# Kernel optimization log

Measured on AMD Instinct MI355X. Metric: run time of the kernel, lower is better.

Reference implementation:

```python
import jax, jax.numpy as jnp
import numpy as np

N_NODES = 50000


def rgcn_conv(x, src, dst, edge_type, W, root, bias):
    """PyG RGCNConv: out[i] = x[i] @ root + bias + sum_r mean_{j in N_r(i)} x[j] @ W[r].
    W: [R, F_in, F_out]. Mean aggregation is per-relation (PyG default aggr='mean')."""
    num_rel = W.shape[0]
    n = x.shape[0]
    out = x @ root + bias
    x_src = x[src]  # [E, F_in] gather once
    for r in range(num_rel):  # small fixed relation count
        mask = (edge_type == r)
        msg = jnp.where(mask[:, None], x_src, 0.0) @ W[r]          # [E, F_out]
        s = jax.ops.segment_sum(msg, dst, num_segments=n)           # [N, F_out]
        c = jax.ops.segment_sum(mask.astype(x.dtype), dst, num_segments=n)  # [N]
        out = out + s / jnp.maximum(c, 1.0)[:, None]
    return out


def setup_inputs() -> dict:
    key = jax.random.key(0)
    ks = jax.random.split(key, 10)
    N, E, F_in, F_hid, F_out, R = N_NODES, 800000, 128, 128, 64, 8
    x = jax.random.normal(ks[0], (N, F_in), dtype=jnp.float32)
    edge_index = jax.random.randint(ks[1], (2, E), 0, N, dtype=jnp.int64)
    edge_type = jax.random.randint(ks[2], (E,), 0, R, dtype=jnp.int64)
    s1 = 1.0 / np.sqrt(F_in)
    s2 = 1.0 / np.sqrt(F_hid)
    W1 = jax.random.normal(ks[3], (R, F_in, F_hid), dtype=jnp.float32) * s1
    root1 = jax.random.normal(ks[4], (F_in, F_hid), dtype=jnp.float32) * s1
    b1 = jnp.zeros((F_hid,), dtype=jnp.float32)
    W2 = jax.random.normal(ks[5], (R, F_hid, F_out), dtype=jnp.float32) * s2
    root2 = jax.random.normal(ks[6], (F_hid, F_out), dtype=jnp.float32) * s2
    b2 = jnp.zeros((F_out,), dtype=jnp.float32)
    return {"x": x, "edge_index": edge_index, "edge_type": edge_type,
            "W1": W1, "root1": root1, "b1": b1,
            "W2": W2, "root2": root2, "b2": b2}


def reference(x, edge_index, edge_type, W1, root1, b1, W2, root2, b2):
    src, dst = edge_index[0], edge_index[1]
    h = jax.nn.relu(rgcn_conv(x, src, dst, edge_type, W1, root1, b1))
    out = rgcn_conv(h, src, dst, edge_type, W2, root2, b2)
    return out
```

## Files before the change

kernel.cpp:

```cpp
#include <hip/hip_runtime.h>

#define N_NODES 50000
#define N_EDGES 800000
#define R_REL   8

#define TNBKT   3125
#define TCAP    512
#define SLAB    4096
#define BINBLK  ((N_EDGES + SLAB - 1) / SLAB)

typedef float  f32x4  __attribute__((ext_vector_type(4)));
typedef __bf16 bf16x8 __attribute__((ext_vector_type(8)));

__device__ __forceinline__ unsigned short f2bf(float f) {
    unsigned int u = __float_as_uint(f);
    u = (u + 0x7FFFu + ((u >> 16) & 1u)) >> 16;
    return (unsigned short)u;
}
__device__ __forceinline__ float bflo(unsigned int u) { return __uint_as_float(u << 16); }
__device__ __forceinline__ float bfhi(unsigned int u) { return __uint_as_float(u & 0xFFFF0000u); }

__device__ __forceinline__ void acc16(float* a, uint4 u0, uint4 u1) {
    a[0]  += bflo(u0.x);   a[1]  += bfhi(u0.x);
    a[2]  += bflo(u0.y);   a[3]  += bfhi(u0.y);
    a[4]  += bflo(u0.z);   a[5]  += bfhi(u0.z);
    a[6]  += bflo(u0.w);   a[7]  += bfhi(u0.w);
    a[8]  += bflo(u1.x);   a[9]  += bfhi(u1.x);
    a[10] += bflo(u1.y);   a[11] += bfhi(u1.y);
    a[12] += bflo(u1.z);   a[13] += bfhi(u1.z);
    a[14] += bflo(u1.w);   a[15] += bfhi(u1.w);
}


#define W1_ELEMS (9 * 128 * 128)
#define W2_ELEMS (9 * 64 * 128)
#define N4       (N_NODES * 32)
#define NB_CVT   ((N4 + 255) / 256)
#define NB_PREP  (BINBLK + NB_CVT)

__global__ __launch_bounds__(256) void k_prep(
    const int* __restrict__ src, const int* __restrict__ dst,
    const int* __restrict__ et, int* __restrict__ gcur,
    unsigned* __restrict__ gbin,
    const float* __restrict__ x, unsigned short* __restrict__ xb,
    const float* __restrict__ root1, const float* __restrict__ W1,
    const float* __restrict__ root2, const float* __restrict__ W2,
    unsigned short* __restrict__ Wt1, unsigned short* __restrict__ Wt2)
{
    __shared__ int hist[TNBKT];
    __shared__ int base[TNBKT];
    const int t = threadIdx.x;

    if (blockIdx.x < BINBLK) {
        const int e0 = blockIdx.x * SLAB;
        for (int i = t; i < TNBKT; i += 256) hist[i] = 0;
        __syncthreads();
#pragma unroll
        for (int i = 0; i < SLAB / 256; ++i) {
            int e = e0 + i * 256 + t;
            if (e < N_EDGES) atomicAdd(&hist[dst[e] >> 4], 1);
        }
        __syncthreads();
        for (int i = t; i < TNBKT; i += 256) {
            int h = hist[i];
            base[i] = (h > 0) ? atomicAdd(&gcur[i], h) : 0;
            hist[i] = 0;
        }
        __syncthreads();
#pragma unroll
        for (int i = 0; i < SLAB / 256; ++i) {
            int e = e0 + i * 256 + t;
            if (e < N_EDGES) {
                int d = dst[e];
                int b = d >> 4;
                int sub = atomicAdd(&hist[b], 1);
                int pos = base[b] + sub;
                unsigned rec = ((unsigned)src[e] << 7) | (unsigned)((d & 15) * 8 + et[e]);
                if (pos < TCAP) gbin[(size_t)b * TCAP + pos] = rec;
            }
        }
        return;
    }

    const int idx = (blockIdx.x - BINBLK) * 256 + t;
    if (idx < N4) {
        float4 v = *(const float4*)(x + (size_t)idx * 4);
        ushort4 o;
        o.x = f2bf(v.x); o.y = f2bf(v.y); o.z = f2bf(v.z); o.w = f2bf(v.w);
        *(ushort4*)(xb + (size_t)idx * 4) = o;
    }
    if (idx < W1_ELEMS) {
        int j    = idx & 7;
        int lane = (idx >> 3) & 63;
        int r    = idx >> 9;
        int nb   = r & 7;
        int r2   = r >> 3;
        int kk   = r2 & 3;
        int seg  = r2 >> 2;
        int k = kk * 32 + (lane >> 4) * 8 + j;
        int n = nb * 16 + (lane & 15);
        float v = (seg == 0) ? root1[k * 128 + n] : W1[((seg - 1) * 128 + k) * 128 + n];
        Wt1[idx] = f2bf(v);
    } else if (idx < W1_ELEMS + W2_ELEMS) {
        int i2   = idx - W1_ELEMS;
        int j    = i2 & 7;
        int lane = (i2 >> 3) & 63;
        int r    = i2 >> 9;
        int nb   = r & 3;
        int r2   = r >> 2;
        int kk   = r2 & 3;
        int seg  = r2 >> 2;
        int k = kk * 32 + (lane >> 4) * 8 + j;
        int n = nb * 16 + (lane & 15);
        float v = (seg == 0) ? root2[k * 64 + n] : W2[((seg - 1) * 128 + k) * 64 + n];
        Wt2[i2] = f2bf(v);
    }
}


template <int FOUT, bool RELU, bool OUT_BF16>
__global__ __launch_bounds__(512) void k_fused(
    const unsigned short* __restrict__ xin,
    const unsigned short* __restrict__ WtP,
    const float* __restrict__ bias,
    const int* __restrict__ gcnt,
    const unsigned* __restrict__ gbin,
    unsigned short* __restrict__ outb,
    float* __restrict__ outf)
{
    constexpr int NBt = FOUT / 16;
    __shared__ __align__(16) unsigned short As0[16][136];
    __shared__ __align__(16) unsigned short As[8][16][136];
    __shared__ unsigned short sorted[TCAP];
    __shared__ int dcnt[128];
    __shared__ int kbeg[128];
    __shared__ int kcur[128];

    const int t = threadIdx.x;
    const int node0 = blockIdx.x * 16;

    if (t < 128) { dcnt[t] = 0; kcur[t] = 0; }
    if (t < 128) {
        const int sr = t >> 3;
        const int sp = t & 7;
        const uint4* s4 = (const uint4*)(xin + (size_t)(node0 + sr) * 128 + sp * 16);
        uint4 r0 = s4[0], r1 = s4[1];
        uint4* d = (uint4*)&As0[sr][sp * 16];
        d[0] = r0; d[1] = r1;
    }
    const int nraw = gcnt[blockIdx.x];
    const int n = nraw < TCAP ? nraw : TCAP;
    unsigned rec = 0;
    if (t < n) rec = gbin[(size_t)blockIdx.x * TCAP + t];
    __syncthreads();

    if (t < n) atomicAdd(&dcnt[rec & 127], 1);
    __syncthreads();

    if (t < 64) {
        int d0 = dcnt[2 * t], d1 = dcnt[2 * t + 1];
        int s = d0 + d1;
        int inc = s;
#pragma unroll
        for (int off = 1; off < 64; off <<= 1) {
            int y = __shfl_up(inc, off, 64);
            if (t >= off) inc += y;
        }
        int excl = inc - s;
        kbeg[2 * t]     = excl;
        kbeg[2 * t + 1] = excl + d0;
    }
    __syncthreads();

    if (t < n) {
        int key = rec & 127;
        int pos = atomicAdd(&kcur[key], 1);
        sorted[kbeg[key] + pos] = (unsigned short)(rec >> 7);
    }
    __syncthreads();

    {
        const int key = t >> 2;
        const int q   = t & 3;
        const int rel = key & 7;
        const int nl  = key >> 3;

        const int beg = kbeg[key];
        const int deg = dcnt[key];
        const int end = beg + deg;

        const unsigned short* bx = xin + q * 32;
        float a[32];
#pragma unroll
        for (int i = 0; i < 32; ++i) a[i] = 0.f;

        int j = beg;
        for (; j + 1 < end; j += 2) {
            int s0 = sorted[j];
            int s1 = sorted[j + 1];
            const uint4* p0 = (const uint4*)(bx + (size_t)s0 * 128);
            const uint4* p1 = (const uint4*)(bx + (size_t)s1 * 128);
            uint4 v0 = p0[0], v1 = p0[1], v2 = p0[2], v3 = p0[3];
            uint4 w0 = p1[0], w1 = p1[1], w2 = p1[2], w3 = p1[3];
            acc16(a, v0, v1);
            acc16(a + 16, v2, v3);
            acc16(a, w0, w1);
            acc16(a + 16, w2, w3);
        }
        if (j < end) {
            int s = sorted[j];
            const uint4* p = (const uint4*)(bx + (size_t)s * 128);
            uint4 v0 = p[0], v1 = p[1], v2 = p[2], v3 = p[3];
            acc16(a, v0, v1);
            acc16(a + 16, v2, v3);
        }

        float scl = 1.f / (float)(deg > 1 ? deg : 1);
        unsigned int pk[16];
#pragma unroll
        for (int i = 0; i < 16; ++i)
            pk[i] = (unsigned int)f2bf(a[i * 2] * scl) |
                    ((unsigned int)f2bf(a[i * 2 + 1] * scl) << 16);
        uint4* G = (uint4*)&As[rel][nl][0];
        const int g0 = q * 4;
        G[(g0 + 0) ^ rel] = make_uint4(pk[0],  pk[1],  pk[2],  pk[3]);
        G[(g0 + 1) ^ rel] = make_uint4(pk[4],  pk[5],  pk[6],  pk[7]);
        G[(g0 + 2) ^ rel] = make_uint4(pk[8],  pk[9],  pk[10], pk[11]);
        G[(g0 + 3) ^ rel] = make_uint4(pk[12], pk[13], pk[14], pk[15]);
    }

    __syncthreads();

    const int lane = t & 63;
    const int w = t >> 6;
    if (w >= NBt) return;
    const int quad = lane >> 4;
    const int tc = lane & 15;

    f32x4 acc = (f32x4){0.f, 0.f, 0.f, 0.f};
    const bf16x8* Bp = (const bf16x8*)WtP;

#pragma unroll
    for (int seg = 0; seg < 9; ++seg) {
        const uint4* Ag = (seg == 0) ? (const uint4*)&As0[tc][0]
                                     : (const uint4*)&As[seg - 1][tc][0];
        const int s = (seg == 0) ? 0 : (seg - 1);
#pragma unroll
        for (int kk = 0; kk < 4; ++kk) {
            bf16x8 af = *(const bf16x8*)(Ag + (((kk << 2) + quad) ^ s));
            bf16x8 bf = Bp[((seg * 4 + kk) * NBt + w) * 64 + lane];
            acc = __builtin_amdgcn_mfma_f32_16x16x32_bf16(af, bf, acc, 0, 0, 0);
        }
    }

    const int col = w * 16 + tc;
    const float bs = bias[col];
#pragma unroll
    for (int i = 0; i < 4; ++i) {
        int r = node0 + quad * 4 + i;
        float v = acc[i] + bs;
        if (RELU) v = fmaxf(v, 0.f);
        if (OUT_BF16) outb[(size_t)r * FOUT + col] = f2bf(v);
        else          outf[(size_t)r * FOUT + col] = v;
    }
}


extern "C" void kernel_launch(void* const* d_in, const int* in_sizes, int n_in,
                              void* d_out, int out_size, void* d_ws, size_t ws_size,
                              hipStream_t stream) {
    const float* x     = (const float*)d_in[0];
    const int*   ei    = (const int*)d_in[1];
    const int*   et    = (const int*)d_in[2];
    const float* W1    = (const float*)d_in[3];
    const float* root1 = (const float*)d_in[4];
    const float* b1    = (const float*)d_in[5];
    const float* W2    = (const float*)d_in[6];
    const float* root2 = (const float*)d_in[7];
    const float* b2    = (const float*)d_in[8];
    float* out = (float*)d_out;

    int* ws = (int*)d_ws;
    int* gcur = ws;
    unsigned* gbin = (unsigned*)(gcur + 3200);
    unsigned short* xb  = (unsigned short*)(gbin + (size_t)TNBKT * TCAP);
    unsigned short* hb  = xb + (size_t)N_NODES * 128;
    unsigned short* Wt1 = hb + (size_t)N_NODES * 128;
    unsigned short* Wt2 = Wt1 + W1_ELEMS;

    const int* esrc = ei;
    const int* edst = ei + N_EDGES;

    hipMemsetAsync(gcur, 0, 3200 * sizeof(int), stream);
    k_prep<<<NB_PREP, 256, 0, stream>>>(esrc, edst, et, gcur, gbin,
                                        x, xb, root1, W1, root2, W2, Wt1, Wt2);

    const int NT = N_NODES / 16;

    k_fused<128, true,  true ><<<NT, 512, 0, stream>>>(xb, Wt1, b1, gcur, gbin, hb, nullptr);
    k_fused<64,  false, false><<<NT, 512, 0, stream>>>(hb, Wt2, b2, gcur, gbin, nullptr, out);
}
```

Baseline: 250.7 us.

## Bucket edges by destination in two passes: coarse then fine

Replaces the single-pass 3125-bucket edge binning with a two-level partition. The first pass bins edges into 196 coarse buckets of 256 nodes using a small shared histogram and few global atomics. A new kernel then splits each coarse bucket into 16 fine buckets and writes per-bucket counts. This cuts the per-block histogram init and scan over 3125 entries and the global atomic contention, at the cost of an extra kernel launch and an extra pass over the edge records.

After: 245.4 us, median of 2. 1.02x faster.

```diff
diff --git a/kernel.cpp b/kernel.cpp
--- a/kernel.cpp
+++ b/kernel.cpp
@@ -4,6 +4,8 @@
 #define N_EDGES 800000
 #define R_REL   8
 
+#define NCB     196
+#define CCAP    5120
 #define TNBKT   3125
 #define TCAP    512
 #define SLAB    4096
@@ -40,31 +42,31 @@
 
 __global__ __launch_bounds__(256) void k_prep(
     const int* __restrict__ src, const int* __restrict__ dst,
-    const int* __restrict__ et, int* __restrict__ gcur,
-    unsigned* __restrict__ gbin,
+    const int* __restrict__ et, int* __restrict__ gcur1,
+    unsigned* __restrict__ cbin,
     const float* __restrict__ x, unsigned short* __restrict__ xb,
     const float* __restrict__ root1, const float* __restrict__ W1,
     const float* __restrict__ root2, const float* __restrict__ W2,
     unsigned short* __restrict__ Wt1, unsigned short* __restrict__ Wt2)
 {
-    __shared__ int hist[TNBKT];
-    __shared__ int base[TNBKT];
+    __shared__ int hist[256];
+    __shared__ int base[256];
     const int t = threadIdx.x;
 
     if (blockIdx.x < BINBLK) {
         const int e0 = blockIdx.x * SLAB;
-        for (int i = t; i < TNBKT; i += 256) hist[i] = 0;
+        hist[t] = 0;
         __syncthreads();
 #pragma unroll
         for (int i = 0; i < SLAB / 256; ++i) {
             int e = e0 + i * 256 + t;
-            if (e < N_EDGES) atomicAdd(&hist[dst[e] >> 4], 1);
+            if (e < N_EDGES) atomicAdd(&hist[dst[e] >> 8], 1);
         }
         __syncthreads();
-        for (int i = t; i < TNBKT; i += 256) {
-            int h = hist[i];
-            base[i] = (h > 0) ? atomicAdd(&gcur[i], h) : 0;
-            hist[i] = 0;
+        {
+            int h = hist[t];
+            base[t] = (h > 0) ? atomicAdd(&gcur1[t], h) : 0;
+            hist[t] = 0;
         }
         __syncthreads();
 #pragma unroll
@@ -72,11 +74,13 @@
             int e = e0 + i * 256 + t;
             if (e < N_EDGES) {
                 int d = dst[e];
-                int b = d >> 4;
+                int b = d >> 8;
                 int sub = atomicAdd(&hist[b], 1);
                 int pos = base[b] + sub;
-                unsigned rec = ((unsigned)src[e] << 7) | (unsigned)((d & 15) * 8 + et[e]);
-                if (pos < TCAP) gbin[(size_t)b * TCAP + pos] = rec;
+                unsigned rec = ((unsigned)src[e] << 11) |
+                               ((unsigned)((d >> 4) & 15) << 7) |
+                               (unsigned)((d & 15) * 8 + et[e]);
+                if (pos < CCAP) cbin[(size_t)b * CCAP + pos] = rec;
             }
         }
         return;
@@ -118,6 +122,35 @@
 }
 
 
+__global__ __launch_bounds__(256) void k_part2(
+    const int* __restrict__ gcur1, const unsigned* __restrict__ cbin,
+    unsigned* __restrict__ gbin, int* __restrict__ gcnt)
+{
+    __shared__ int cur[16];
+    const int t = threadIdx.x;
+    const int b = blockIdx.x;
+    if (t < 16) cur[t] = 0;
+    __syncthreads();
+    const int nraw = gcur1[b];
+    const int n = nraw < CCAP ? nraw : CCAP;
+    const unsigned* rp = cbin + (size_t)b * CCAP;
+    for (int j = t; j < n; j += 256) {
+        unsigned rec = rp[j];
+        int lt = (rec >> 7) & 15;
+        int sub = atomicAdd(&cur[lt], 1);
+        if (sub < TCAP) {
+            unsigned outrec = ((rec >> 11) << 7) | (rec & 127);
+            gbin[(size_t)(b * 16 + lt) * TCAP + sub] = outrec;
+        }
+    }
+    __syncthreads();
+    if (t < 16) {
+        int c = cur[t];
+        gcnt[b * 16 + t] = c < TCAP ? c : TCAP;
+    }
+}
+
+
 template <int FOUT, bool RELU, bool OUT_BF16>
 __global__ __launch_bounds__(512) void k_fused(
     const unsigned short* __restrict__ xin,
@@ -281,8 +314,10 @@
     float* out = (float*)d_out;
 
     int* ws = (int*)d_ws;
-    int* gcur = ws;
-    unsigned* gbin = (unsigned*)(gcur + 3200);
+    int* gcur1 = ws;
+    int* gcnt  = ws + 256;
+    unsigned* cbin = (unsigned*)(ws + 3456);
+    unsigned* gbin = cbin + (size_t)NCB * CCAP;
     unsigned short* xb  = (unsigned short*)(gbin + (size_t)TNBKT * TCAP);
     unsigned short* hb  = xb + (size_t)N_NODES * 128;
     unsigned short* Wt1 = hb + (size_t)N_NODES * 128;
@@ -291,12 +326,13 @@
     const int* esrc = ei;
     const int* edst = ei + N_EDGES;
 
-    hipMemsetAsync(gcur, 0, 3200 * sizeof(int), stream);
-    k_prep<<<NB_PREP, 256, 0, stream>>>(esrc, edst, et, gcur, gbin,
+    hipMemsetAsync(gcur1, 0, 256 * sizeof(int), stream);
+    k_prep<<<NB_PREP, 256, 0, stream>>>(esrc, edst, et, gcur1, cbin,
                                         x, xb, root1, W1, root2, W2, Wt1, Wt2);
+    k_part2<<<NCB, 256, 0, stream>>>(gcur1, cbin, gbin, gcnt);
 
     const int NT = N_NODES / 16;
 
-    k_fused<128, true,  true ><<<NT, 512, 0, stream>>>(xb, Wt1, b1, gcur, gbin, hb, nullptr);
-    k_fused<64,  false, false><<<NT, 512, 0, stream>>>(hb, Wt2, b2, gcur, gbin, nullptr, out);
-}
+    k_fused<128, true,  true ><<<NT, 512, 0, stream>>>(xb, Wt1, b1, gcnt, gbin, hb, nullptr);
+    k_fused<64,  false, false><<<NT, 512, 0, stream>>>(hb, Wt2, b2, gcnt, gbin, nullptr, out);
+}
```
